# Kernel tuning notes

Measured on AMD Instinct MI355X. Metric: run time of the kernel, lower is better.

Reference implementation:

```python
import jax, jax.numpy as jnp
import numpy as np

HUMAN_CONF = 0.7
KP_CONF = 0.5
NMS_THR = 0.5


def _cxcywh_to_xyxy(b):
    cx, cy, w, h = b[..., 0], b[..., 1], b[..., 2], b[..., 3]
    return jnp.stack([cx - 0.5 * w, cy - 0.5 * h, cx + 0.5 * w, cy + 0.5 * h], axis=-1)


def _iou_matrix(boxes):  # [Q,4] xyxy -> [Q,Q]
    area = jnp.maximum(boxes[:, 2] - boxes[:, 0], 0) * jnp.maximum(boxes[:, 3] - boxes[:, 1], 0)
    lt = jnp.maximum(boxes[:, None, :2], boxes[None, :, :2])
    rb = jnp.minimum(boxes[:, None, 2:], boxes[None, :, 2:])
    wh = jnp.maximum(rb - lt, 0)
    inter = wh[..., 0] * wh[..., 1]
    union = area[:, None] + area[None, :] - inter
    return inter / jnp.maximum(union, 1e-9)


def _nms(boxes, scores, valid, thr):
    # Greedy NMS over score-sorted boxes; invalid boxes never kept.
    Q = scores.shape[0]
    order = jnp.argsort(jnp.where(valid, scores, -jnp.inf))[::-1]
    b, v = boxes[order], valid[order]
    iou = _iou_matrix(b)
    idxs = jnp.arange(Q)

    def body(sup, i):
        keep_i = v[i] & jnp.logical_not(sup[i])
        sup = sup | (keep_i & (iou[i] > thr) & (idxs != i))
        return sup, keep_i

    _, keeps = jax.lax.scan(body, jnp.zeros(Q, bool), idxs)
    return jnp.zeros(Q, bool).at[order].set(keeps)


def _roi_kps(hm, box, sx, sy):
    # hm: [K,H,W] float, box: [4] int32 (xyxy in image coords).
    # Masked full-map argmax == ROI-crop argmax of the original (outside = -inf).
    K, H, W = hm.shape
    x1 = jnp.maximum((box[0].astype(jnp.float32) * sx).astype(jnp.int32), 0)
    y1 = jnp.maximum((box[1].astype(jnp.float32) * sy).astype(jnp.int32), 0)
    x2 = jnp.minimum((box[2].astype(jnp.float32) * sx).astype(jnp.int32) + 1, W)
    y2 = jnp.minimum((box[3].astype(jnp.float32) * sy).astype(jnp.int32) + 1, H)
    xs, ys = jnp.arange(W), jnp.arange(H)
    mask = ((ys >= y1) & (ys < y2))[:, None] & ((xs >= x1) & (xs < x2))[None, :]
    flat = jnp.where(mask[None], hm, -jnp.inf).reshape(K, -1)
    max_vals = flat.max(-1)
    idx = flat.argmax(-1)
    col = (idx % W).astype(jnp.float32)
    row = (idx // W).astype(jnp.float32)
    kps = jnp.stack([col / sx, row / sy, max_vals], -1)  # [K,3]
    ok = (x2 > x1) & (y2 > y1)
    return jnp.where(ok, kps, 0.0)


def setup_inputs() -> dict:
    key = jax.random.key(0)
    k1, k2, k3 = jax.random.split(key, 3)
    B, Q, K, Hh, Wh = 4, 100, 17, 128, 128
    return {
        "human_logits": jax.random.normal(k1, (B, Q, 2), jnp.float32) * 2.0,
        "pred_boxes": jax.random.uniform(k2, (B, Q, 4), jnp.float32),
        "pred_heatmaps": jax.random.normal(k3, (B, K, Hh, Wh), jnp.float32),
        "img_h": 512,
        "img_w": 512,
    }


def reference(human_logits, pred_boxes, pred_heatmaps, img_h, img_w):
    K, Hh, Wh = pred_heatmaps.shape[1:]
    prob = jax.nn.softmax(human_logits, -1)
    scores = prob.max(-1)          # [B,Q]
    labels = prob.argmax(-1)       # [B,Q]
    scale = jnp.array([img_w, img_h, img_w, img_h], jnp.float32)
    boxes = _cxcywh_to_xyxy(pred_boxes) * scale  # [B,Q,4] image coords
    valid = (labels == 0) & (scores >= HUMAN_CONF)
    keep = jax.vmap(lambda b, s, v: _nms(b, s, v, NMS_THR))(boxes, scores, valid)  # [B,Q] bool
    boxes_int = boxes.astype(jnp.int32)
    sx, sy = Wh / img_w, Hh / img_h
    kps = jax.vmap(lambda hm, bx: jax.vmap(lambda b: _roi_kps(hm, b, sx, sy))(bx))(
        pred_heatmaps, boxes_int)  # [B,Q,K,3]
    conf = kps[..., 2]
    kps = kps.at[..., 2].set(jnp.where(conf < KP_CONF, 0.0, conf))
    keep_f = keep.astype(jnp.float32)
    scores_out = scores * keep_f
    kps_out = kps * keep_f[:, :, None, None]
    boxes_out = boxes_int * keep[:, :, None]
    return scores_out, boxes_out, kps_out, keep
```

## Files before the change

### kernel.cpp

```cpp
#include <hip/hip_runtime.h>
#include <cmath>
#include <cfloat>

constexpr int NB = 4;
constexpr int NQ = 100;
constexpr int NK = 17;
constexpr int NH = 128;
constexpr int NW = 128;

constexpr float HUMAN_CONF = 0.7f;
constexpr float KP_CONF    = 0.5f;
constexpr float NMS_THR    = 0.5f;

constexpr int OFF_BOXES = NB * NQ;
constexpr int OFF_KPS   = NB * NQ * 5;
constexpr int OFF_KEEP  = NB * NQ * 5 + NB * NQ * NK * 3;

constexpr int NBLK = 1024;
constexpr int WAVES_PER_BATCH = (NBLK / NB) * 2;

__global__ __launch_bounds__(128) void fused_kernel(
    const float* __restrict__ logits,
    const float* __restrict__ pboxes,
    const float* __restrict__ hm,
    const int* __restrict__ img_h_p,
    const int* __restrict__ img_w_p,
    float* __restrict__ out)
{
    const int blk = blockIdx.x;
    const int t   = threadIdx.x;
    const int b   = blk & 3;
    const int sub = blk >> 2;

    __shared__ float sbx[NQ][4];
    __shared__ float ssc[NQ];
    __shared__ unsigned char sval[NQ];
    __shared__ int   sorder[NQ];
    __shared__ float sortb[NQ][4];
    __shared__ float sarea[NQ];
    __shared__ unsigned char ssv[NQ];
    __shared__ unsigned long long smask0[NQ], smask1[NQ];
    __shared__ unsigned long long skmask[2];
    __shared__ unsigned long long svb[2];
    __shared__ int sqpack[NQ];

    float4 wv4 = make_float4(0.f, 0.f, 0.f, 0.f);
    const int  line = blk * 128 + t;
    const bool doW  = line < (NB * NK * NH * NW) / 16;
    if (doW) wv4 = ((const float4*)hm)[line * 4];

    const float iw = (float)img_w_p[0];
    const float ih = (float)img_h_p[0];
    const float sxl = (float)NW / iw;
    const float syl = (float)NH / ih;

    if (t < NQ) {
        const float l0 = logits[(b * NQ + t) * 2 + 0];
        const float l1 = logits[(b * NQ + t) * 2 + 1];
        const float m  = fmaxf(l0, l1);
        const float e0 = expf(l0 - m);
        const float e1 = expf(l1 - m);
        const float score = fmaxf(e0, e1) / (e0 + e1);
        const bool  lab0  = (l0 >= l1);

        const float cx = pboxes[(b * NQ + t) * 4 + 0];
        const float cy = pboxes[(b * NQ + t) * 4 + 1];
        const float w  = pboxes[(b * NQ + t) * 4 + 2];
        const float h  = pboxes[(b * NQ + t) * 4 + 3];
        sbx[t][0] = (cx - 0.5f * w) * iw;
        sbx[t][1] = (cy - 0.5f * h) * ih;
        sbx[t][2] = (cx + 0.5f * w) * iw;
        sbx[t][3] = (cy + 0.5f * h) * ih;
        ssc[t]  = score;
        sval[t] = (lab0 && score >= HUMAN_CONF) ? 1 : 0;
    }
    __syncthreads();

    if (t < NQ) {
        const float key = sval[t] ? ssc[t] : -INFINITY;
        int rank = 0;
        for (int j = 0; j < NQ; ++j) {
            const float kj = sval[j] ? ssc[j] : -INFINITY;
            if (kj > key || (kj == key && j > t)) rank++;
        }
        sorder[rank] = t;
    }
    __syncthreads();

    if (t < NQ) {
        const int oi = sorder[t];
        const float x1 = sbx[oi][0], y1 = sbx[oi][1], x2 = sbx[oi][2], y2 = sbx[oi][3];
        sortb[t][0] = x1; sortb[t][1] = y1; sortb[t][2] = x2; sortb[t][3] = y2;
        sarea[t] = fmaxf(x2 - x1, 0.0f) * fmaxf(y2 - y1, 0.0f);
        ssv[t]   = sval[oi];
    }
    __syncthreads();

    if (t < NQ) {
        unsigned long long m0 = 0ull, m1 = 0ull;
        const float ax1 = sortb[t][0], ay1 = sortb[t][1], ax2 = sortb[t][2], ay2 = sortb[t][3];
        const float aa = sarea[t];
        for (int j = 0; j < NQ; ++j) {
            const float lx = fmaxf(ax1, sortb[j][0]);
            const float ly = fmaxf(ay1, sortb[j][1]);
            const float rx = fminf(ax2, sortb[j][2]);
            const float ry = fminf(ay2, sortb[j][3]);
            const float wv = fmaxf(rx - lx, 0.0f);
            const float hv = fmaxf(ry - ly, 0.0f);
            const float inter = wv * hv;
            const float uni = aa + sarea[j] - inter;
            const float iou = inter / fmaxf(uni, 1e-9f);
            if (iou > NMS_THR) {
                if (j < 64) m0 |= 1ull << j; else m1 |= 1ull << (j - 64);
            }
        }
        smask0[t] = m0; smask1[t] = m1;
    }

    {
        const bool sv = (t < NQ) ? (ssv[t] != 0) : false;
        const unsigned long long vb = __ballot(sv);
        if ((t & 63) == 0) svb[t >> 6] = vb;
    }
    __syncthreads();

    if (t == 0) {
        unsigned long long rem0 = svb[0], rem1 = svb[1];
        unsigned long long k0 = 0ull, k1 = 0ull;
        while (rem0 | rem1) {
            int i;
            unsigned long long bit0 = 0ull, bit1 = 0ull;
            if (rem0) { i = __builtin_ctzll(rem0); bit0 = 1ull << i; }
            else      { const int j = __builtin_ctzll(rem1); i = 64 + j; bit1 = 1ull << j; }
            k0 |= bit0; k1 |= bit1;
            rem0 &= ~(smask0[i] | bit0);
            rem1 &= ~(smask1[i] | bit1);
        }
        skmask[0] = k0; skmask[1] = k1;
    }
    __syncthreads();

    if (t < NQ) {
        const int oi = sorder[t];
        const int kp = (t < 64) ? (int)((skmask[0] >> t) & 1ull)
                                : (int)((skmask[1] >> (t - 64)) & 1ull);

        const int bi0 = (int)sbx[oi][0];
        const int bi1 = (int)sbx[oi][1];
        const int bi2 = (int)sbx[oi][2];
        const int bi3 = (int)sbx[oi][3];

        const int x1i = max((int)((float)bi0 * sxl), 0);
        const int y1i = max((int)((float)bi1 * syl), 0);
        const int x2i = min((int)((float)bi2 * sxl) + 1, NW);
        const int y2i = min((int)((float)bi3 * syl) + 1, NH);
        const bool live = kp && (x2i > x1i) && (y2i > y1i);

        sqpack[oi] = live ? (x1i | (y1i << 8) | (x2i << 16) | (y2i << 24)) : 0;

        if (sub == 0) {
            const int gi = b * NQ + oi;
            out[gi] = ssc[oi] * (float)kp;
            out[OFF_BOXES + gi * 4 + 0] = (float)(bi0 * kp);
            out[OFF_BOXES + gi * 4 + 1] = (float)(bi1 * kp);
            out[OFF_BOXES + gi * 4 + 2] = (float)(bi2 * kp);
            out[OFF_BOXES + gi * 4 + 3] = (float)(bi3 * kp);
            out[OFF_KEEP + gi] = (float)kp;
        }
    }
    __syncthreads();

    if (doW) asm volatile("" :: "v"(wv4.x), "v"(wv4.y), "v"(wv4.z), "v"(wv4.w));

    const int lane = t & 63;
    const int wvid = sub * 2 + (t >> 6);

    for (int item = wvid; item < NQ * NK; item += WAVES_PER_BATCH) {
        const int q = item / NK;
        const int k = item - q * NK;
        const int gi = b * NQ + q;
        float* kout = out + OFF_KPS + (size_t)gi * (NK * 3) + k * 3;

        const int pack = sqpack[q];
        if (pack == 0) {
            if (lane < 3) kout[lane] = 0.0f;
            continue;
        }

        const int x1 = pack & 255;
        const int y1 = (pack >> 8) & 255;
        const int x2 = (pack >> 16) & 255;
        const int y2 = (pack >> 24) & 255;

        const float4* __restrict__ b4 =
            (const float4*)(hm + (size_t)(b * NK + k) * (NH * NW));

        const int xa     = x1 & ~3;
        const int C4     = (x2 - xa + 3) >> 2;
        const int R      = y2 - y1;
        const int total4 = R * C4;
        const unsigned M = (C4 > 1) ? (0xFFFFFFFFu / (unsigned)C4 + 1u) : 0u;

        float best = -INFINITY;
        int   bidx = 0x7fffffff;

        auto proc = [&](int idx, float4 v) {
            const int row = (C4 == 1) ? idx : (int)__umulhi((unsigned)idx, M);
            const int xb  = xa + (idx - row * C4) * 4;
            const int g   = (y1 + row) * NW + xb;
            const float v0 = (xb + 0 >= x1 && xb + 0 < x2) ? v.x : -INFINITY;
            const float v1 = (xb + 1 >= x1 && xb + 1 < x2) ? v.y : -INFINITY;
            const float v2 = (xb + 2 >= x1 && xb + 2 < x2) ? v.z : -INFINITY;
            const float v3 = (xb + 3 < x2) ? v.w : -INFINITY;
            if (v0 > best) { best = v0; bidx = g + 0; }
            if (v1 > best) { best = v1; bidx = g + 1; }
            if (v2 > best) { best = v2; bidx = g + 2; }
            if (v3 > best) { best = v3; bidx = g + 3; }
        };
        auto caddr = [&](int idx) {
            const int row = (C4 == 1) ? idx : (int)__umulhi((unsigned)idx, M);
            return (y1 + row) * (NW / 4) + (xa >> 2) + (idx - row * C4);
        };

        int idx = lane;
        for (; idx + 192 < total4; idx += 256) {
            const int a0 = caddr(idx), a1 = caddr(idx + 64), a2 = caddr(idx + 128), a3 = caddr(idx + 192);
            const float4 v0 = b4[a0];
            const float4 v1 = b4[a1];
            const float4 v2 = b4[a2];
            const float4 v3 = b4[a3];
            proc(idx, v0);
            proc(idx + 64, v1);
            proc(idx + 128, v2);
            proc(idx + 192, v3);
        }
        for (; idx < total4; idx += 64) proc(idx, b4[caddr(idx)]);

        for (int off = 32; off >= 1; off >>= 1) {
            const float ov = __shfl_down(best, off);
            const int   oi = __shfl_down(bidx, off);
            if (ov > best || (ov == best && oi < bidx)) { best = ov; bidx = oi; }
        }

        if (lane == 0) {
            const int col = bidx & (NW - 1);
            const int row = bidx >> 7;
            float conf = best;
            if (conf < KP_CONF) conf = 0.0f;
            kout[0] = (float)col / sxl;
            kout[1] = (float)row / syl;
            kout[2] = conf;
        }
    }
}

extern "C" void kernel_launch(void* const* d_in, const int* in_sizes, int n_in,
                              void* d_out, int out_size, void* d_ws, size_t ws_size,
                              hipStream_t stream) {
    const float* logits = (const float*)d_in[0];
    const float* pboxes = (const float*)d_in[1];
    const float* hm     = (const float*)d_in[2];
    const int*   img_h  = (const int*)d_in[3];
    const int*   img_w  = (const int*)d_in[4];
    float* out = (float*)d_out;

    fused_kernel<<<NBLK, 128, 0, stream>>>(logits, pboxes, hm, img_h, img_w, out);
}
```

Baseline: 105.8 us.

## Streamline NMS prologue: keep boxes in registers, compact valid boxes, shuffle-based greedy scan

Restructures the per-block NMS prologue. Box and score data now stay in registers and are loaded with vector loads. Only valid boxes are scattered into a compact sorted array, and the IoU loop runs over that valid count only. The greedy suppression loop reads mask rows through wave shuffles instead of shared memory. This removes two barriers and the redundant shared-memory staging, trading them for more per-thread register state and a wave-wide serial loop. Since the heatmap argmax loop dominates runtime, the gain in the prologue may be small.

```diff
diff --git a/kernel.cpp b/kernel.cpp
--- a/kernel.cpp
+++ b/kernel.cpp
@@ -32,16 +32,11 @@
     const int b   = blk & 3;
     const int sub = blk >> 2;
 
-    __shared__ float sbx[NQ][4];
-    __shared__ float ssc[NQ];
-    __shared__ unsigned char sval[NQ];
-    __shared__ int   sorder[NQ];
-    __shared__ float sortb[NQ][4];
-    __shared__ float sarea[NQ];
-    __shared__ unsigned char ssv[NQ];
+    __shared__ float  skey[NQ];
+    __shared__ float4 srtb[104];
     __shared__ unsigned long long smask0[NQ], smask1[NQ];
+    __shared__ unsigned long long svb[2];
     __shared__ unsigned long long skmask[2];
-    __shared__ unsigned long long svb[2];
     __shared__ int sqpack[NQ];
 
     float4 wv4 = make_float4(0.f, 0.f, 0.f, 0.f);
@@ -54,78 +49,88 @@
     const float sxl = (float)NW / iw;
     const float syl = (float)NH / ih;
 
+    if (t < 104) srtb[t] = make_float4(0.f, 0.f, 0.f, 0.f);
+
+    float score = 0.f, x1 = 0.f, y1 = 0.f, x2 = 0.f, y2 = 0.f;
+    bool valid = false;
     if (t < NQ) {
-        const float l0 = logits[(b * NQ + t) * 2 + 0];
-        const float l1 = logits[(b * NQ + t) * 2 + 1];
-        const float m  = fmaxf(l0, l1);
-        const float e0 = expf(l0 - m);
-        const float e1 = expf(l1 - m);
-        const float score = fmaxf(e0, e1) / (e0 + e1);
-        const bool  lab0  = (l0 >= l1);
-
-        const float cx = pboxes[(b * NQ + t) * 4 + 0];
-        const float cy = pboxes[(b * NQ + t) * 4 + 1];
-        const float w  = pboxes[(b * NQ + t) * 4 + 2];
-        const float h  = pboxes[(b * NQ + t) * 4 + 3];
-        sbx[t][0] = (cx - 0.5f * w) * iw;
-        sbx[t][1] = (cy - 0.5f * h) * ih;
-        sbx[t][2] = (cx + 0.5f * w) * iw;
-        sbx[t][3] = (cy + 0.5f * h) * ih;
-        ssc[t]  = score;
-        sval[t] = (lab0 && score >= HUMAN_CONF) ? 1 : 0;
-    }
-    __syncthreads();
-
+        const float2 lg = ((const float2*)logits)[b * NQ + t];
+        const float m  = fmaxf(lg.x, lg.y);
+        const float e0 = expf(lg.x - m);
+        const float e1 = expf(lg.y - m);
+        score = fmaxf(e0, e1) / (e0 + e1);
+        const bool lab0 = (lg.x >= lg.y);
+
+        const float4 pb = ((const float4*)pboxes)[b * NQ + t];
+        x1 = (pb.x - 0.5f * pb.z) * iw;
+        y1 = (pb.y - 0.5f * pb.w) * ih;
+        x2 = (pb.x + 0.5f * pb.z) * iw;
+        y2 = (pb.y + 0.5f * pb.w) * ih;
+
+        valid = lab0 && (score >= HUMAN_CONF);
+        skey[t] = valid ? score : -INFINITY;
+    }
+    {
+        const unsigned long long vb = __ballot(valid);
+        if ((t & 63) == 0) svb[t >> 6] = vb;
+    }
+    __syncthreads();
+
+    const int V = __popcll(svb[0]) + __popcll(svb[1]);
+
+    int r = 0;
     if (t < NQ) {
-        const float key = sval[t] ? ssc[t] : -INFINITY;
-        int rank = 0;
-        for (int j = 0; j < NQ; ++j) {
-            const float kj = sval[j] ? ssc[j] : -INFINITY;
-            if (kj > key || (kj == key && j > t)) rank++;
-        }
-        sorder[rank] = t;
-    }
-    __syncthreads();
-
-    if (t < NQ) {
-        const int oi = sorder[t];
-        const float x1 = sbx[oi][0], y1 = sbx[oi][1], x2 = sbx[oi][2], y2 = sbx[oi][3];
-        sortb[t][0] = x1; sortb[t][1] = y1; sortb[t][2] = x2; sortb[t][3] = y2;
-        sarea[t] = fmaxf(x2 - x1, 0.0f) * fmaxf(y2 - y1, 0.0f);
-        ssv[t]   = sval[oi];
-    }
-    __syncthreads();
-
-    if (t < NQ) {
+        const float key = valid ? score : -INFINITY;
+        for (int j = 0; j < NQ; j += 4) {
+            const float a0 = skey[j + 0];
+            const float a1 = skey[j + 1];
+            const float a2 = skey[j + 2];
+            const float a3 = skey[j + 3];
+            r += (a0 > key || (a0 == key && (j + 0) > t)) ? 1 : 0;
+            r += (a1 > key || (a1 == key && (j + 1) > t)) ? 1 : 0;
+            r += (a2 > key || (a2 == key && (j + 2) > t)) ? 1 : 0;
+            r += (a3 > key || (a3 == key && (j + 3) > t)) ? 1 : 0;
+        }
+        if (valid) srtb[r] = make_float4(x1, y1, x2, y2);
+    }
+    __syncthreads();
+
+    if (valid) {
         unsigned long long m0 = 0ull, m1 = 0ull;
-        const float ax1 = sortb[t][0], ay1 = sortb[t][1], ax2 = sortb[t][2], ay2 = sortb[t][3];
-        const float aa = sarea[t];
-        for (int j = 0; j < NQ; ++j) {
-            const float lx = fmaxf(ax1, sortb[j][0]);
-            const float ly = fmaxf(ay1, sortb[j][1]);
-            const float rx = fminf(ax2, sortb[j][2]);
-            const float ry = fminf(ay2, sortb[j][3]);
-            const float wv = fmaxf(rx - lx, 0.0f);
-            const float hv = fmaxf(ry - ly, 0.0f);
-            const float inter = wv * hv;
-            const float uni = aa + sarea[j] - inter;
-            const float iou = inter / fmaxf(uni, 1e-9f);
-            if (iou > NMS_THR) {
-                if (j < 64) m0 |= 1ull << j; else m1 |= 1ull << (j - 64);
+        const float aa = fmaxf(x2 - x1, 0.f) * fmaxf(y2 - y1, 0.f);
+        const int Vp = (V + 3) & ~3;
+        for (int j = 0; j < Vp; j += 4) {
+            #pragma unroll
+            for (int u = 0; u < 4; ++u) {
+                const float4 bb = srtb[j + u];
+                const float ba = fmaxf(bb.z - bb.x, 0.f) * fmaxf(bb.w - bb.y, 0.f);
+                const float lx = fmaxf(x1, bb.x);
+                const float ly = fmaxf(y1, bb.y);
+                const float rx = fminf(x2, bb.z);
+                const float ry = fminf(y2, bb.w);
+                const float wv = fmaxf(rx - lx, 0.f);
+                const float hv = fmaxf(ry - ly, 0.f);
+                const float inter = wv * hv;
+                const float uni = aa + ba - inter;
+                const float iou = inter / fmaxf(uni, 1e-9f);
+                if (iou > NMS_THR) {
+                    const int jj = j + u;
+                    if (jj < 64) m0 |= 1ull << jj; else m1 |= 1ull << (jj - 64);
+                }
             }
         }
-        smask0[t] = m0; smask1[t] = m1;
-    }
-
-    {
-        const bool sv = (t < NQ) ? (ssv[t] != 0) : false;
-        const unsigned long long vb = __ballot(sv);
-        if ((t & 63) == 0) svb[t >> 6] = vb;
-    }
-    __syncthreads();
-
-    if (t == 0) {
-        unsigned long long rem0 = svb[0], rem1 = svb[1];
+        smask0[r] = m0; smask1[r] = m1;
+    }
+    __syncthreads();
+
+    if (t < 64) {
+        const unsigned long long rm0 = smask0[t];
+        const unsigned long long rm1 = smask1[t];
+
+        unsigned long long rem0 = (V >= 64) ? ~0ull : ((1ull << V) - 1ull);
+        unsigned long long rem1 = 0ull;
+        if (V > 64) { const int v1 = V - 64; rem1 = (v1 >= 64) ? ~0ull : ((1ull << v1) - 1ull); }
+
         unsigned long long k0 = 0ull, k1 = 0ull;
         while (rem0 | rem1) {
             int i;
@@ -133,22 +138,32 @@
             if (rem0) { i = __builtin_ctzll(rem0); bit0 = 1ull << i; }
             else      { const int j = __builtin_ctzll(rem1); i = 64 + j; bit1 = 1ull << j; }
             k0 |= bit0; k1 |= bit1;
-            rem0 &= ~(smask0[i] | bit0);
-            rem1 &= ~(smask1[i] | bit1);
-        }
-        skmask[0] = k0; skmask[1] = k1;
+            unsigned long long row0, row1;
+            if (i < 64) {
+                row0 = __shfl(rm0, i);
+                row1 = __shfl(rm1, i);
+            } else {
+                row0 = smask0[i];
+                row1 = smask1[i];
+            }
+            rem0 &= ~(row0 | bit0);
+            rem1 &= ~(row1 | bit1);
+        }
+        if (t == 0) { skmask[0] = k0; skmask[1] = k1; }
     }
     __syncthreads();
 
     if (t < NQ) {
-        const int oi = sorder[t];
-        const int kp = (t < 64) ? (int)((skmask[0] >> t) & 1ull)
-                                : (int)((skmask[1] >> (t - 64)) & 1ull);
-
-        const int bi0 = (int)sbx[oi][0];
-        const int bi1 = (int)sbx[oi][1];
-        const int bi2 = (int)sbx[oi][2];
-        const int bi3 = (int)sbx[oi][3];
+        const unsigned long long k0s = skmask[0];
+        const unsigned long long k1s = skmask[1];
+        int kp = 0;
+        if (valid) kp = (r < 64) ? (int)((k0s >> r) & 1ull)
+                                 : (int)((k1s >> (r - 64)) & 1ull);
+
+        const int bi0 = (int)x1;
+        const int bi1 = (int)y1;
+        const int bi2 = (int)x2;
+        const int bi3 = (int)y2;
 
         const int x1i = max((int)((float)bi0 * sxl), 0);
         const int y1i = max((int)((float)bi1 * syl), 0);
@@ -156,11 +171,11 @@
         const int y2i = min((int)((float)bi3 * syl) + 1, NH);
         const bool live = kp && (x2i > x1i) && (y2i > y1i);
 
-        sqpack[oi] = live ? (x1i | (y1i << 8) | (x2i << 16) | (y2i << 24)) : 0;
+        sqpack[t] = live ? (x1i | (y1i << 8) | (x2i << 16) | (y2i << 24)) : 0;
 
         if (sub == 0) {
-            const int gi = b * NQ + oi;
-            out[gi] = ssc[oi] * (float)kp;
+            const int gi = b * NQ + t;
+            out[gi] = score * (float)kp;
             out[OFF_BOXES + gi * 4 + 0] = (float)(bi0 * kp);
             out[OFF_BOXES + gi * 4 + 1] = (float)(bi1 * kp);
             out[OFF_BOXES + gi * 4 + 2] = (float)(bi2 * kp);
@@ -187,17 +202,17 @@
             continue;
         }
 
-        const int x1 = pack & 255;
-        const int y1 = (pack >> 8) & 255;
-        const int x2 = (pack >> 16) & 255;
-        const int y2 = (pack >> 24) & 255;
+        const int x1r = pack & 255;
+        const int y1r = (pack >> 8) & 255;
+        const int x2r = (pack >> 16) & 255;
+        const int y2r = (pack >> 24) & 255;
 
         const float4* __restrict__ b4 =
             (const float4*)(hm + (size_t)(b * NK + k) * (NH * NW));
 
-        const int xa     = x1 & ~3;
-        const int C4     = (x2 - xa + 3) >> 2;
-        const int R      = y2 - y1;
+        const int xa     = x1r & ~3;
+        const int C4     = (x2r - xa + 3) >> 2;
+        const int R      = y2r - y1r;
         const int total4 = R * C4;
         const unsigned M = (C4 > 1) ? (0xFFFFFFFFu / (unsigned)C4 + 1u) : 0u;
 
@@ -207,11 +222,11 @@
         auto proc = [&](int idx, float4 v) {
             const int row = (C4 == 1) ? idx : (int)__umulhi((unsigned)idx, M);
             const int xb  = xa + (idx - row * C4) * 4;
-            const int g   = (y1 + row) * NW + xb;
-            const float v0 = (xb + 0 >= x1 && xb + 0 < x2) ? v.x : -INFINITY;
-            const float v1 = (xb + 1 >= x1 && xb + 1 < x2) ? v.y : -INFINITY;
-            const float v2 = (xb + 2 >= x1 && xb + 2 < x2) ? v.z : -INFINITY;
-            const float v3 = (xb + 3 < x2) ? v.w : -INFINITY;
+            const int g   = (y1r + row) * NW + xb;
+            const float v0 = (xb + 0 >= x1r && xb + 0 < x2r) ? v.x : -INFINITY;
+            const float v1 = (xb + 1 >= x1r && xb + 1 < x2r) ? v.y : -INFINITY;
+            const float v2 = (xb + 2 >= x1r && xb + 2 < x2r) ? v.z : -INFINITY;
+            const float v3 = (xb + 3 < x2r) ? v.w : -INFINITY;
             if (v0 > best) { best = v0; bidx = g + 0; }
             if (v1 > best) { best = v1; bidx = g + 1; }
             if (v2 > best) { best = v2; bidx = g + 2; }
@@ -219,7 +234,7 @@
         };
         auto caddr = [&](int idx) {
             const int row = (C4 == 1) ? idx : (int)__umulhi((unsigned)idx, M);
-            return (y1 + row) * (NW / 4) + (xa >> 2) + (idx - row * C4);
+            return (y1r + row) * (NW / 4) + (xa >> 2) + (idx - row * C4);
         };
 
         int idx = lane;
```

New measurement: 96.83 us. 1.09x faster.
